# Kernel tuning notes

Hardware: AMD Instinct MI355X
Metric: run time of the kernel (lower is better)

## Reference

```python
import jax, jax.numpy as jnp
import numpy as np

DIM = 512
NUM_HEADS = 8
HEAD_DIM = DIM // NUM_HEADS


def setup_inputs() -> dict:
    key = jax.random.key(0)
    k_x, k_qkv, k_p = jax.random.split(key, 3)
    b, n, c = 8, 4096, DIM
    x = jax.random.normal(k_x, (b, n, c), dtype=jnp.float32)
    # xavier_uniform for Linear(dim, 3*dim): limit = sqrt(6/(in+out))
    lim_qkv = float(np.sqrt(6.0 / (c + 3 * c)))
    w_qkv = jax.random.uniform(k_qkv, (c, 3 * c), dtype=jnp.float32, minval=-lim_qkv, maxval=lim_qkv)
    b_qkv = jnp.zeros((3 * c,), dtype=jnp.float32)
    lim_p = float(np.sqrt(6.0 / (c + c)))
    w_p = jax.random.uniform(k_p, (c, c), dtype=jnp.float32, minval=-lim_p, maxval=lim_p)
    b_p = jnp.zeros((c,), dtype=jnp.float32)
    temperature = jnp.full((NUM_HEADS, 1, 1), 1.0 / np.sqrt(HEAD_DIM), dtype=jnp.float32)
    return {"x": x, "w_qkv": w_qkv, "b_qkv": b_qkv, "w_p": w_p, "b_p": b_p,
            "temperature": temperature}


def reference(x, w_qkv, b_qkv, w_p, b_p, temperature):
    b, n, c = x.shape
    h, d = NUM_HEADS, HEAD_DIM
    qkv = x @ w_qkv + b_qkv                      # [b, n, 3c]
    q, k, v = jnp.split(qkv, 3, axis=-1)         # each [b, n, c]
    # -> [b, h, n, d]
    q = q.reshape(b, n, h, d).transpose(0, 2, 1, 3)
    k = k.reshape(b, n, h, d).transpose(0, 2, 1, 3)
    v = v.reshape(b, n, h, d).transpose(0, 2, 1, 3)
    # channel attention: d x d score matrix, reduced over tokens n
    scores = jnp.einsum('bhnd,bhne->bhde', q, k) * temperature  # [b,h,d,d]
    attn = jax.nn.softmax(scores, axis=-1)
    # y = attn @ v^T then permute -> [b, n, h, d]
    y = jnp.einsum('bhde,bhne->bnhd', attn, v).reshape(b, n, c)
    return y @ w_p + b_p
```

## Files before the change

### kernel.cpp

```cpp
#include <hip/hip_runtime.h>

typedef __attribute__((ext_vector_type(8))) short s16x8;
typedef __attribute__((ext_vector_type(4))) short s16x4;
typedef __attribute__((ext_vector_type(4))) float fx4;

__device__ inline unsigned short f2bf(float f) {
  unsigned u = __float_as_uint(f);
  u += 0x7fffu + ((u >> 16) & 1u);
  return (unsigned short)(u >> 16);
}
__device__ inline float bf2f(unsigned short s) {
  return __uint_as_float(((unsigned)s) << 16);
}

#define GLDS16(gp, lp) \
  __builtin_amdgcn_global_load_lds((const __attribute__((address_space(1))) void*)(gp), \
                                   (__attribute__((address_space(3))) void*)(lp), 16, 0, 0)

__global__ __launch_bounds__(256) void cast_x_k(const float* __restrict__ x,
                                                unsigned short* __restrict__ xb) {
  int i = (blockIdx.x * 256 + threadIdx.x) * 8;
  fx4 a = *(const fx4*)&x[i];
  fx4 b = *(const fx4*)&x[i + 4];
  s16x8 o;
  o[0] = (short)f2bf(a[0]); o[1] = (short)f2bf(a[1]);
  o[2] = (short)f2bf(a[2]); o[3] = (short)f2bf(a[3]);
  o[4] = (short)f2bf(b[0]); o[5] = (short)f2bf(b[1]);
  o[6] = (short)f2bf(b[2]); o[7] = (short)f2bf(b[3]);
  *(s16x8*)&xb[i] = o;
}

__global__ __launch_bounds__(256) void twqkv_k(const float* __restrict__ w,
                                               unsigned short* __restrict__ wT) {
  int o = blockIdx.x * 256 + threadIdx.x;
  int j = o >> 9, kk = o & 511;
  wT[o] = f2bf(w[kk * 1536 + j]);
}

__global__ __launch_bounds__(256) void cast_wp_k(const float* __restrict__ w,
                                                 unsigned short* __restrict__ wb) {
  int o = blockIdx.x * 256 + threadIdx.x;
  wb[o] = f2bf(w[o]);
}

template <int MODE>
__global__ __launch_bounds__(256, 4) void gemm_k(
    const unsigned short* __restrict__ A, const unsigned short* __restrict__ BT,
    const float* __restrict__ bias,
    unsigned short* __restrict__ qo, unsigned short* __restrict__ ko,
    unsigned short* __restrict__ vo, float* __restrict__ outp) {
  __shared__ alignas(16) unsigned short As[2][128 * 32];
  __shared__ alignas(16) unsigned short Bs[2][128 * 32];
  int tid = threadIdx.x, wave = tid >> 6, lane = tid & 63;
  int l15 = lane & 15, l16 = lane >> 4;
  int wr = wave >> 1, wc = wave & 1;

  int nwg = (MODE == 0) ? 3072 : 1024;
  int cpx = nwg >> 3;
  int bid = (blockIdx.x & 7) * cpx + (blockIdx.x >> 3);

  int mt, nt, bb = 0;
  if (MODE == 0) { mt = bid / 12; nt = bid % 12; }
  else { bb = bid >> 7; int r = bid & 127; mt = r >> 2; nt = r & 3; }
  const unsigned short* Ab = A + (MODE == 0 ? (size_t)0 : (size_t)bb * 4096 * 512);
  const unsigned short* Bb = BT + (MODE == 0 ? (size_t)0 : (size_t)bb * 512 * 512);
  int row0 = mt * 128, col0 = nt * 128;

  fx4 acc[4][4];
#pragma unroll
  for (int i = 0; i < 4; ++i)
#pragma unroll
    for (int j = 0; j < 4; ++j) acc[i][j] = (fx4){0.f, 0.f, 0.f, 0.f};

  int smr = wave * 16 + (lane >> 2);
  int skk = (((lane & 3) ^ ((lane >> 3) & 3))) * 8;
  const unsigned short* agp = Ab + (size_t)(row0 + smr) * 512 + skk;
  const unsigned short* bgp = Bb + (size_t)(col0 + smr) * 512 + skk;
  int ldsoff = wave * 512;

#define STAGE(buf, kt_)                                        \
  do {                                                         \
    int k0_ = (kt_) * 32;                                      \
    GLDS16(agp + k0_, &As[buf][ldsoff]);                       \
    GLDS16(agp + 64 * 512 + k0_, &As[buf][ldsoff + 2048]);     \
    GLDS16(bgp + k0_, &Bs[buf][ldsoff]);                       \
    GLDS16(bgp + 64 * 512 + k0_, &Bs[buf][ldsoff + 2048]);     \
  } while (0)

  STAGE(0, 0);
  asm volatile("s_waitcnt vmcnt(0)" ::: "memory");
  __builtin_amdgcn_s_barrier();

  int g = (l15 >> 1) & 3;
  int pa = (l16 ^ g) << 3;

  for (int kt = 0; kt < 16; ++kt) {
    int cur = kt & 1;
    if (kt < 15) STAGE(cur ^ 1, kt + 1);

    s16x8 af[4], bf[4];
#pragma unroll
    for (int mi = 0; mi < 4; ++mi)
      af[mi] = *(const s16x8*)&As[cur][(wr * 64 + mi * 16 + l15) * 32 + pa];
#pragma unroll
    for (int nj = 0; nj < 4; ++nj)
      bf[nj] = *(const s16x8*)&Bs[cur][(wc * 64 + nj * 16 + l15) * 32 + pa];
#pragma unroll
    for (int mi = 0; mi < 4; ++mi)
#pragma unroll
      for (int nj = 0; nj < 4; ++nj)
        acc[mi][nj] = __builtin_amdgcn_mfma_f32_16x16x32_bf16(af[mi], bf[nj], acc[mi][nj], 0, 0, 0);

    asm volatile("s_waitcnt vmcnt(0)" ::: "memory");
    __builtin_amdgcn_s_barrier();
  }
#undef STAGE

  int crow0 = row0 + wr * 64;
  int ccol0 = col0 + wc * 64;
  if (MODE == 0) {
    int seg = ccol0 >> 9;
#pragma unroll
    for (int mi = 0; mi < 4; ++mi)
#pragma unroll
      for (int nj = 0; nj < 4; ++nj) {
        int gc = ccol0 + nj * 16 + l15;
        float bsv = bias[gc];
#pragma unroll
        for (int r = 0; r < 4; ++r) {
          int gr = crow0 + mi * 16 + l16 * 4 + r;
          unsigned short o = f2bf(acc[mi][nj][r] + bsv);
          int b_ = gr >> 12, n_ = gr & 4095;
          if (seg == 0) {
            qo[((((size_t)b_ * 8 + (gc >> 6)) * 4096 + n_) << 6) + (gc & 63)] = o;
          } else if (seg == 1) {
            int c2 = gc - 512;
            ko[((((size_t)b_ * 8 + (c2 >> 6)) * 4096 + n_) << 6) + (c2 & 63)] = o;
          } else {
            vo[((size_t)gr << 9) + (gc - 1024)] = o;
          }
        }
      }
  } else {
#pragma unroll
    for (int mi = 0; mi < 4; ++mi)
#pragma unroll
      for (int nj = 0; nj < 4; ++nj) {
        int gc = ccol0 + nj * 16 + l15;
        float bsv = bias[gc];
#pragma unroll
        for (int r = 0; r < 4; ++r) {
          int gr = crow0 + mi * 16 + l16 * 4 + r;
          outp[(((size_t)bb * 4096 + gr) << 9) + gc] = acc[mi][nj][r] + bsv;
        }
      }
  }
}

__global__ __launch_bounds__(256) void scores_partial_k(const unsigned short* __restrict__ q,
                                                        const unsigned short* __restrict__ k,
                                                        float* __restrict__ sp) {
  __shared__ alignas(16) float qs[64 * 64];
  __shared__ alignas(16) float ks[64 * 64];
  int bid = blockIdx.x;
  int bh = bid >> 3, seg = bid & 7;
  const unsigned short* qb = q + ((size_t)bh * 4096 + seg * 512) * 64;
  const unsigned short* kb = k + ((size_t)bh * 4096 + seg * 512) * 64;
  int tid = threadIdx.x;
  int dg = tid >> 4, eg = tid & 15;
  float acc[4][4] = {{0.f}};
  for (int ch = 0; ch < 8; ++ch) {
    __syncthreads();
    for (int r = 0; r < 4; ++r) {
      int idx = r * 1024 + tid * 4;
      s16x4 qv = *(const s16x4*)&qb[ch * 4096 + idx];
      s16x4 kv = *(const s16x4*)&kb[ch * 4096 + idx];
      fx4 qf = {bf2f((unsigned short)qv[0]), bf2f((unsigned short)qv[1]),
                bf2f((unsigned short)qv[2]), bf2f((unsigned short)qv[3])};
      fx4 kf = {bf2f((unsigned short)kv[0]), bf2f((unsigned short)kv[1]),
                bf2f((unsigned short)kv[2]), bf2f((unsigned short)kv[3])};
      *(fx4*)&qs[idx] = qf;
      *(fx4*)&ks[idx] = kf;
    }
    __syncthreads();
    for (int n = 0; n < 64; ++n) {
      fx4 qv4 = *(const fx4*)&qs[n * 64 + dg * 4];
      fx4 kv4 = *(const fx4*)&ks[n * 64 + eg * 4];
      for (int i = 0; i < 4; ++i)
        for (int j = 0; j < 4; ++j) acc[i][j] += qv4[i] * kv4[j];
    }
  }
  float* o = sp + (size_t)bid * 4096;
  for (int i = 0; i < 4; ++i)
    for (int j = 0; j < 4; ++j) o[(dg * 4 + i) * 64 + eg * 4 + j] = acc[i][j];
}

__global__ __launch_bounds__(256) void softmax_weff_k(const float* __restrict__ sp,
                                                      const unsigned short* __restrict__ wpb,
                                                      const float* __restrict__ temp,
                                                      unsigned short* __restrict__ weffT) {
  __shared__ alignas(16) float S[64 * 64];
  __shared__ alignas(16) unsigned short wps[64 * 128];
  int bh = blockIdx.x >> 2, jblk = blockIdx.x & 3;
  int b = bh >> 3, h = bh & 7;
  int tid = threadIdx.x;
  float tval = temp[h];
  for (int i = tid * 4; i < 4096; i += 1024) {
    fx4 s = {0.f, 0.f, 0.f, 0.f};
    for (int seg = 0; seg < 8; ++seg) {
      fx4 v4 = *(const fx4*)&sp[((size_t)(bh * 8 + seg)) * 4096 + i];
      s += v4;
    }
    s *= tval;
    *(fx4*)&S[i] = s;
  }
  for (int i = tid * 8; i < 8192; i += 2048) {
    int d = i >> 7, c = i & 127;
    *(s16x8*)&wps[i] = *(const s16x8*)&wpb[(size_t)(h * 64 + d) * 512 + jblk * 128 + c];
  }
  __syncthreads();
  if (tid < 64) {
    float* row = &S[tid * 64];
    float mx = row[0];
    for (int e = 1; e < 64; ++e) mx = fmaxf(mx, row[e]);
    float sum = 0.f;
    for (int e = 0; e < 64; ++e) { float p = __expf(row[e] - mx); row[e] = p; sum += p; }
    float inv = 1.f / sum;
    for (int e = 0; e < 64; ++e) row[e] *= inv;
  }
  __syncthreads();
  int jg = tid >> 4, eg = tid & 15;
  int j0 = jg * 8;
  float a[4][8];
  for (int i = 0; i < 4; ++i)
    for (int j = 0; j < 8; ++j) a[i][j] = 0.f;
  for (int d = 0; d < 64; ++d) {
    fx4 at = *(const fx4*)&S[d * 64 + eg * 4];
    s16x8 wv = *(const s16x8*)&wps[d * 128 + j0];
    float wf[8];
    for (int j = 0; j < 8; ++j) wf[j] = bf2f((unsigned short)wv[j]);
    for (int i = 0; i < 4; ++i)
      for (int j = 0; j < 8; ++j) a[i][j] += at[i] * wf[j];
  }
  int jglob = jblk * 128 + j0;
  for (int j = 0; j < 8; ++j)
    for (int i = 0; i < 4; ++i)
      weffT[(((size_t)b * 512 + jglob + j) << 9) + h * 64 + eg * 4 + i] = f2bf(a[i][j]);
}

extern "C" void kernel_launch(void* const* d_in, const int* in_sizes, int n_in,
                              void* d_out, int out_size, void* d_ws, size_t ws_size,
                              hipStream_t stream) {
  const float* x      = (const float*)d_in[0];
  const float* w_qkv  = (const float*)d_in[1];
  const float* b_qkv  = (const float*)d_in[2];
  const float* w_p    = (const float*)d_in[3];
  const float* b_p    = (const float*)d_in[4];
  const float* temp   = (const float*)d_in[5];
  float* out = (float*)d_out;
  char* ws = (char*)d_ws;

  unsigned short* xb    = (unsigned short*)(ws + 0);
  float*          sp    = (float*)(ws + 0);
  unsigned short* weffT = (unsigned short*)(ws + 8388608);
  unsigned short* wqkvT = (unsigned short*)(ws + 33554432);
  unsigned short* wpb   = (unsigned short*)(ws + 35127296);
  unsigned short* qb    = (unsigned short*)(ws + 35651584);
  unsigned short* kb    = (unsigned short*)(ws + 69206016);
  unsigned short* vb    = (unsigned short*)(ws + 102760448);

  cast_x_k<<<8192, 256, 0, stream>>>(x, xb);
  twqkv_k<<<3072, 256, 0, stream>>>(w_qkv, wqkvT);
  cast_wp_k<<<1024, 256, 0, stream>>>(w_p, wpb);
  gemm_k<0><<<3072, 256, 0, stream>>>(xb, wqkvT, b_qkv, qb, kb, vb, nullptr);
  scores_partial_k<<<512, 256, 0, stream>>>(qb, kb, sp);
  softmax_weff_k<<<256, 256, 0, stream>>>(sp, wpb, temp, weffT);
  gemm_k<1><<<1024, 256, 0, stream>>>(vb, weffT, b_p, nullptr, nullptr, nullptr, out);
}
```

Baseline: 171.3 us.

## Reassociate channel attention to avoid materializing Q and V projections

Rewrites the pipeline algebraically. It computes K^T via a GEMM, then X^T K per batch as a split-K GEMM, and forms the scores as Wq^T (X^T K) with bias corrections derived from column sums of x. V is never materialized: softmax·Wp is folded with Wv into a per-batch combined weight, so the final output is a single x @ Wcomb GEMM. The intent is to drop the large Q/V projection GEMMs and their memory traffic. In exchange it adds transposes of x, split-K partial buffers, atomics for the bias terms, and numerics that differ from the original order of operations.

```diff
diff --git a/kernel.cpp b/kernel.cpp
--- a/kernel.cpp
+++ b/kernel.cpp
@@ -18,53 +18,149 @@
                                    (__attribute__((address_space(3))) void*)(lp), 16, 0, 0)
 
 __global__ __launch_bounds__(256) void cast_x_k(const float* __restrict__ x,
-                                                unsigned short* __restrict__ xb) {
-  int i = (blockIdx.x * 256 + threadIdx.x) * 8;
-  fx4 a = *(const fx4*)&x[i];
-  fx4 b = *(const fx4*)&x[i + 4];
-  s16x8 o;
-  o[0] = (short)f2bf(a[0]); o[1] = (short)f2bf(a[1]);
-  o[2] = (short)f2bf(a[2]); o[3] = (short)f2bf(a[3]);
-  o[4] = (short)f2bf(b[0]); o[5] = (short)f2bf(b[1]);
-  o[6] = (short)f2bf(b[2]); o[7] = (short)f2bf(b[3]);
-  *(s16x8*)&xb[i] = o;
-}
-
-__global__ __launch_bounds__(256) void twqkv_k(const float* __restrict__ w,
-                                               unsigned short* __restrict__ wT) {
-  int o = blockIdx.x * 256 + threadIdx.x;
-  int j = o >> 9, kk = o & 511;
-  wT[o] = f2bf(w[kk * 1536 + j]);
-}
-
-__global__ __launch_bounds__(256) void cast_wp_k(const float* __restrict__ w,
-                                                 unsigned short* __restrict__ wb) {
-  int o = blockIdx.x * 256 + threadIdx.x;
-  wb[o] = f2bf(w[o]);
+                                                unsigned short* __restrict__ xb,
+                                                unsigned short* __restrict__ xT,
+                                                float* __restrict__ s_part) {
+  __shared__ unsigned short lt[64 * 66];
+  __shared__ float red[64 * 4];
+  int blk = blockIdx.x;
+  int b = blk >> 9, r = blk & 511, nt = r >> 3, ct = r & 7;
+  int n0 = nt * 64, c0 = ct * 64;
+  int t = threadIdx.x;
+  int rn = t >> 2, seg = (t & 3) * 16;
+  const float* xp = x + ((size_t)b * 4096 + n0 + rn) * 512 + c0 + seg;
+  fx4 v0 = *(const fx4*)&xp[0], v1 = *(const fx4*)&xp[4];
+  fx4 v2 = *(const fx4*)&xp[8], v3 = *(const fx4*)&xp[12];
+  unsigned short h[16];
+  h[0]=f2bf(v0[0]); h[1]=f2bf(v0[1]); h[2]=f2bf(v0[2]); h[3]=f2bf(v0[3]);
+  h[4]=f2bf(v1[0]); h[5]=f2bf(v1[1]); h[6]=f2bf(v1[2]); h[7]=f2bf(v1[3]);
+  h[8]=f2bf(v2[0]); h[9]=f2bf(v2[1]); h[10]=f2bf(v2[2]); h[11]=f2bf(v2[3]);
+  h[12]=f2bf(v3[0]); h[13]=f2bf(v3[1]); h[14]=f2bf(v3[2]); h[15]=f2bf(v3[3]);
+  unsigned short* xbo = xb + ((size_t)b * 4096 + n0 + rn) * 512 + c0 + seg;
+  *(s16x8*)&xbo[0] = *(s16x8*)&h[0];
+  *(s16x8*)&xbo[8] = *(s16x8*)&h[8];
+#pragma unroll
+  for (int k = 0; k < 16; ++k) lt[(seg + k) * 66 + rn] = h[k];
+  __syncthreads();
+  {
+    int c = t & 63, q = t >> 6;
+    float p = 0.f;
+#pragma unroll
+    for (int i = 0; i < 16; ++i) p += bf2f(lt[c * 66 + q * 16 + i]);
+    red[c * 4 + q] = p;
+  }
+  __syncthreads();
+  if (t < 64) {
+    float s = red[t * 4] + red[t * 4 + 1] + red[t * 4 + 2] + red[t * 4 + 3];
+    s_part[((size_t)(b * 64 + nt)) * 512 + c0 + t] = s;
+  }
+  int c = t >> 2, nseg = (t & 3) * 16;
+  unsigned short* xto = xT + ((size_t)b * 512 + c0 + c) * 4096 + n0 + nseg;
+  *(s16x8*)&xto[0] = *(s16x8*)&lt[c * 66 + nseg];
+  *(s16x8*)&xto[8] = *(s16x8*)&lt[c * 66 + nseg + 8];
+}
+
+__global__ __launch_bounds__(256) void wk_t_k(const float* __restrict__ w,
+                                              unsigned short* __restrict__ wkT) {
+  __shared__ unsigned short lt[64 * 66];
+  int blk = blockIdx.x;
+  int rt = blk >> 3, ct = blk & 7;
+  int t = threadIdx.x;
+  int rn = t >> 2, seg = (t & 3) * 16;
+  const float* wp = w + (size_t)(ct * 64 + rn) * 1536 + 512 + rt * 64 + seg;
+#pragma unroll
+  for (int k = 0; k < 16; ++k) lt[(seg + k) * 66 + rn] = f2bf(wp[k]);
+  __syncthreads();
+  int j = t >> 2, nseg = (t & 3) * 16;
+  unsigned short* o = wkT + (size_t)(rt * 64 + j) * 512 + ct * 64 + nseg;
+  *(s16x8*)&o[0] = *(s16x8*)&lt[j * 66 + nseg];
+  *(s16x8*)&o[8] = *(s16x8*)&lt[j * 66 + nseg + 8];
+}
+
+__global__ __launch_bounds__(256) void wvwp_k(const float* __restrict__ w,
+                                              const float* __restrict__ wp,
+                                              unsigned short* __restrict__ wvb,
+                                              unsigned short* __restrict__ wpb) {
+  int blk = blockIdx.x, t = threadIdx.x;
+  if (blk < 128) {
+    int o = blk * 2048 + t * 8;
+    int c = o >> 9, e = o & 511;
+    const float* src = w + (size_t)c * 1536 + 1024 + e;
+    unsigned short h[8];
+#pragma unroll
+    for (int i = 0; i < 8; ++i) h[i] = f2bf(src[i]);
+    *(s16x8*)&wvb[o] = *(s16x8*)&h[0];
+  } else {
+    int o = (blk - 128) * 2048 + t * 8;
+    unsigned short h[8];
+#pragma unroll
+    for (int i = 0; i < 8; ++i) h[i] = f2bf(wp[o + i]);
+    *(s16x8*)&wpb[o] = *(s16x8*)&h[0];
+  }
+}
+
+__global__ __launch_bounds__(256) void ub_k(const float* __restrict__ s_part,
+                                            const float* __restrict__ w,
+                                            const float* __restrict__ b_p,
+                                            float* __restrict__ u,
+                                            float* __restrict__ bias_out) {
+  __shared__ float sb[128];
+  int b = blockIdx.x >> 2, cq = blockIdx.x & 3;
+  int t = threadIdx.x;
+  if (t < 128) {
+    float a = 0.f;
+    for (int nt = 0; nt < 64; ++nt)
+      a += s_part[((size_t)(b * 64 + nt)) * 512 + cq * 128 + t];
+    sb[t] = a;
+  }
+  __syncthreads();
+  float ua0 = 0.f, ua1 = 0.f, ua2 = 0.f, ua3 = 0.f;
+  for (int c = 0; c < 128; ++c) {
+    float sc = sb[c];
+    const float* wr = w + (size_t)(cq * 128 + c) * 1536;
+    ua0 += sc * wr[t];
+    ua1 += sc * wr[t + 256];
+    ua2 += sc * wr[t + 512];
+    ua3 += sc * wr[t + 768];
+  }
+  atomicAdd(&u[b * 1024 + t], ua0);
+  atomicAdd(&u[b * 1024 + t + 256], ua1);
+  atomicAdd(&u[b * 1024 + t + 512], ua2);
+  atomicAdd(&u[b * 1024 + t + 768], ua3);
+  if (cq == 0) {
+    bias_out[b * 512 + t] = b_p[t];
+    bias_out[b * 512 + 256 + t] = b_p[256 + t];
+  }
 }
 
 template <int MODE>
 __global__ __launch_bounds__(256, 4) void gemm_k(
-    const unsigned short* __restrict__ A, const unsigned short* __restrict__ BT,
-    const float* __restrict__ bias,
-    unsigned short* __restrict__ qo, unsigned short* __restrict__ ko,
-    unsigned short* __restrict__ vo, float* __restrict__ outp) {
+    const unsigned short* __restrict__ A0, const unsigned short* __restrict__ B0,
+    const float* __restrict__ bias, unsigned short* __restrict__ obf,
+    float* __restrict__ of32) {
+  constexpr int LD = (MODE == 1) ? 4096 : 512;
+  constexpr int KSTEPS = (MODE == 1) ? 32 : 16;
+  constexpr int NWG = (MODE == 0) ? 1024 : (MODE == 1) ? 512 : (MODE == 2) ? 128 : 1024;
   __shared__ alignas(16) unsigned short As[2][128 * 32];
   __shared__ alignas(16) unsigned short Bs[2][128 * 32];
   int tid = threadIdx.x, wave = tid >> 6, lane = tid & 63;
   int l15 = lane & 15, l16 = lane >> 4;
   int wr = wave >> 1, wc = wave & 1;
 
-  int nwg = (MODE == 0) ? 3072 : 1024;
-  int cpx = nwg >> 3;
-  int bid = (blockIdx.x & 7) * cpx + (blockIdx.x >> 3);
-
-  int mt, nt, bb = 0;
-  if (MODE == 0) { mt = bid / 12; nt = bid % 12; }
-  else { bb = bid >> 7; int r = bid & 127; mt = r >> 2; nt = r & 3; }
-  const unsigned short* Ab = A + (MODE == 0 ? (size_t)0 : (size_t)bb * 4096 * 512);
-  const unsigned short* Bb = BT + (MODE == 0 ? (size_t)0 : (size_t)bb * 512 * 512);
-  int row0 = mt * 128, col0 = nt * 128;
+  int bid = (blockIdx.x & 7) * (NWG >> 3) + (blockIdx.x >> 3);
+  int b = 0, mt = 0, nt = 0, ks = 0;
+  if (MODE == 0) { b = bid >> 7; int r = bid & 127; mt = r >> 5; nt = r & 31; }
+  else if (MODE == 1) { ks = bid >> 7; int r = bid & 127; b = r >> 4; mt = (r >> 2) & 3; nt = r & 3; }
+  else if (MODE == 2) { b = bid >> 4; mt = (bid >> 2) & 3; nt = bid & 3; }
+  else { b = bid >> 7; int r = bid & 127; mt = r >> 2; nt = r & 3; }
+
+  const unsigned short* Ab;
+  const unsigned short* Bb;
+  if (MODE == 0) { Ab = A0 + (size_t)mt * 128 * 512; Bb = B0 + ((size_t)b * 4096 + nt * 128) * 512; }
+  else if (MODE == 1) { Ab = A0 + ((size_t)b * 512 + mt * 128) * 4096 + ks * 1024;
+                        Bb = B0 + ((size_t)b * 512 + nt * 128) * 4096 + ks * 1024; }
+  else if (MODE == 2) { Ab = A0 + ((size_t)b * 512 + mt * 128) * 512; Bb = B0 + (size_t)nt * 128 * 512; }
+  else { Ab = A0 + ((size_t)b * 4096 + mt * 128) * 512; Bb = B0 + ((size_t)b * 512 + nt * 128) * 512; }
 
   fx4 acc[4][4];
 #pragma unroll
@@ -74,17 +170,17 @@
 
   int smr = wave * 16 + (lane >> 2);
   int skk = (((lane & 3) ^ ((lane >> 3) & 3))) * 8;
-  const unsigned short* agp = Ab + (size_t)(row0 + smr) * 512 + skk;
-  const unsigned short* bgp = Bb + (size_t)(col0 + smr) * 512 + skk;
+  const unsigned short* agp = Ab + (size_t)smr * LD + skk;
+  const unsigned short* bgp = Bb + (size_t)smr * LD + skk;
   int ldsoff = wave * 512;
 
-#define STAGE(buf, kt_)                                        \
-  do {                                                         \
-    int k0_ = (kt_) * 32;                                      \
-    GLDS16(agp + k0_, &As[buf][ldsoff]);                       \
-    GLDS16(agp + 64 * 512 + k0_, &As[buf][ldsoff + 2048]);     \
-    GLDS16(bgp + k0_, &Bs[buf][ldsoff]);                       \
-    GLDS16(bgp + 64 * 512 + k0_, &Bs[buf][ldsoff + 2048]);     \
+#define STAGE(buf, kt_)                                          \
+  do {                                                           \
+    int k0_ = (kt_) * 32;                                        \
+    GLDS16(agp + k0_, &As[buf][ldsoff]);                         \
+    GLDS16(agp + (size_t)64 * LD + k0_, &As[buf][ldsoff + 2048]);\
+    GLDS16(bgp + k0_, &Bs[buf][ldsoff]);                         \
+    GLDS16(bgp + (size_t)64 * LD + k0_, &Bs[buf][ldsoff + 2048]);\
   } while (0)
 
   STAGE(0, 0);
@@ -94,9 +190,9 @@
   int g = (l15 >> 1) & 3;
   int pa = (l16 ^ g) << 3;
 
-  for (int kt = 0; kt < 16; ++kt) {
+  for (int kt = 0; kt < KSTEPS; ++kt) {
     int cur = kt & 1;
-    if (kt < 15) STAGE(cur ^ 1, kt + 1);
+    if (kt < KSTEPS - 1) STAGE(cur ^ 1, kt + 1);
 
     s16x8 af[4], bf[4];
 #pragma unroll
@@ -116,136 +212,123 @@
   }
 #undef STAGE
 
-  int crow0 = row0 + wr * 64;
-  int ccol0 = col0 + wc * 64;
-  if (MODE == 0) {
-    int seg = ccol0 >> 9;
-#pragma unroll
-    for (int mi = 0; mi < 4; ++mi)
-#pragma unroll
-      for (int nj = 0; nj < 4; ++nj) {
-        int gc = ccol0 + nj * 16 + l15;
-        float bsv = bias[gc];
-#pragma unroll
-        for (int r = 0; r < 4; ++r) {
-          int gr = crow0 + mi * 16 + l16 * 4 + r;
-          unsigned short o = f2bf(acc[mi][nj][r] + bsv);
-          int b_ = gr >> 12, n_ = gr & 4095;
-          if (seg == 0) {
-            qo[((((size_t)b_ * 8 + (gc >> 6)) * 4096 + n_) << 6) + (gc & 63)] = o;
-          } else if (seg == 1) {
-            int c2 = gc - 512;
-            ko[((((size_t)b_ * 8 + (c2 >> 6)) * 4096 + n_) << 6) + (c2 & 63)] = o;
-          } else {
-            vo[((size_t)gr << 9) + (gc - 1024)] = o;
-          }
+  int R0 = mt * 128 + wr * 64, C0 = nt * 128 + wc * 64;
+#pragma unroll
+  for (int mi = 0; mi < 4; ++mi)
+#pragma unroll
+    for (int nj = 0; nj < 4; ++nj) {
+      int gc = C0 + nj * 16 + l15;
+#pragma unroll
+      for (int r = 0; r < 4; ++r) {
+        int gr = R0 + mi * 16 + l16 * 4 + r;
+        float val = acc[mi][nj][r];
+        if (MODE == 0) {
+          obf[((size_t)(b * 512 + gr)) * 4096 + gc] = f2bf(val + bias[gr]);
+        } else if (MODE == 1) {
+          of32[((size_t)((ks * 8 + b) * 512 + gr)) * 512 + gc] = val;
+        } else if (MODE == 2) {
+          obf[((size_t)(b * 512 + gr)) * 512 + gc] = f2bf(val);
+        } else {
+          of32[((size_t)(b * 4096 + gr)) * 512 + gc] = val + bias[b * 512 + gc];
         }
       }
-  } else {
-#pragma unroll
-    for (int mi = 0; mi < 4; ++mi)
-#pragma unroll
-      for (int nj = 0; nj < 4; ++nj) {
-        int gc = ccol0 + nj * 16 + l15;
-        float bsv = bias[gc];
-#pragma unroll
-        for (int r = 0; r < 4; ++r) {
-          int gr = crow0 + mi * 16 + l16 * 4 + r;
-          outp[(((size_t)bb * 4096 + gr) << 9) + gc] = acc[mi][nj][r] + bsv;
-        }
-      }
-  }
-}
-
-__global__ __launch_bounds__(256) void scores_partial_k(const unsigned short* __restrict__ q,
-                                                        const unsigned short* __restrict__ k,
-                                                        float* __restrict__ sp) {
-  __shared__ alignas(16) float qs[64 * 64];
-  __shared__ alignas(16) float ks[64 * 64];
-  int bid = blockIdx.x;
-  int bh = bid >> 3, seg = bid & 7;
-  const unsigned short* qb = q + ((size_t)bh * 4096 + seg * 512) * 64;
-  const unsigned short* kb = k + ((size_t)bh * 4096 + seg * 512) * 64;
+    }
+}
+
+__global__ __launch_bounds__(256) void scores_k(
+    const float* __restrict__ Ppart, const float* __restrict__ w_qkv,
+    const float* __restrict__ b_qkv, const float* __restrict__ u,
+    const float* __restrict__ temp, const unsigned short* __restrict__ wpb,
+    unsigned short* __restrict__ weffT, float* __restrict__ bias_out) {
+  __shared__ alignas(16) float Ps[64 * 64];
+  __shared__ alignas(16) float Ws[64 * 64];
+  __shared__ alignas(16) float Ss[64 * 64];
+  __shared__ alignas(16) unsigned short wps[64 * 128];
+  int bh = blockIdx.x;
+  int b = bh >> 3, h = bh & 7;
   int tid = threadIdx.x;
   int dg = tid >> 4, eg = tid & 15;
   float acc[4][4] = {{0.f}};
-  for (int ch = 0; ch < 8; ++ch) {
+  for (int cch = 0; cch < 8; ++cch) {
     __syncthreads();
-    for (int r = 0; r < 4; ++r) {
-      int idx = r * 1024 + tid * 4;
-      s16x4 qv = *(const s16x4*)&qb[ch * 4096 + idx];
-      s16x4 kv = *(const s16x4*)&kb[ch * 4096 + idx];
-      fx4 qf = {bf2f((unsigned short)qv[0]), bf2f((unsigned short)qv[1]),
-                bf2f((unsigned short)qv[2]), bf2f((unsigned short)qv[3])};
-      fx4 kf = {bf2f((unsigned short)kv[0]), bf2f((unsigned short)kv[1]),
-                bf2f((unsigned short)kv[2]), bf2f((unsigned short)kv[3])};
-      *(fx4*)&qs[idx] = qf;
-      *(fx4*)&ks[idx] = kf;
+    for (int p = 0; p < 4; ++p) {
+      int idx = p * 1024 + tid * 4;
+      int cr = idx >> 6, ce = idx & 63;
+      size_t base = ((size_t)(cch * 64 + cr)) * 512 + h * 64 + ce;
+      fx4 v = {0.f, 0.f, 0.f, 0.f};
+#pragma unroll
+      for (int kk = 0; kk < 4; ++kk)
+        v += *(const fx4*)&Ppart[(size_t)(kk * 8 + b) * 262144 + base];
+      *(fx4*)&Ps[idx] = v;
+      *(fx4*)&Ws[idx] = *(const fx4*)&w_qkv[(size_t)(cch * 64 + cr) * 1536 + h * 64 + ce];
     }
     __syncthreads();
-    for (int n = 0; n < 64; ++n) {
-      fx4 qv4 = *(const fx4*)&qs[n * 64 + dg * 4];
-      fx4 kv4 = *(const fx4*)&ks[n * 64 + eg * 4];
+    for (int cc = 0; cc < 64; ++cc) {
+      fx4 wv = *(const fx4*)&Ws[cc * 64 + dg * 4];
+      fx4 pv = *(const fx4*)&Ps[cc * 64 + eg * 4];
+#pragma unroll
       for (int i = 0; i < 4; ++i)
-        for (int j = 0; j < 4; ++j) acc[i][j] += qv4[i] * kv4[j];
-    }
-  }
-  float* o = sp + (size_t)bid * 4096;
+#pragma unroll
+        for (int j = 0; j < 4; ++j) acc[i][j] += wv[i] * pv[j];
+    }
+  }
+  float tval = temp[h];
+  __syncthreads();
+#pragma unroll
   for (int i = 0; i < 4; ++i)
-    for (int j = 0; j < 4; ++j) o[(dg * 4 + i) * 64 + eg * 4 + j] = acc[i][j];
-}
-
-__global__ __launch_bounds__(256) void softmax_weff_k(const float* __restrict__ sp,
-                                                      const unsigned short* __restrict__ wpb,
-                                                      const float* __restrict__ temp,
-                                                      unsigned short* __restrict__ weffT) {
-  __shared__ alignas(16) float S[64 * 64];
-  __shared__ alignas(16) unsigned short wps[64 * 128];
-  int bh = blockIdx.x >> 2, jblk = blockIdx.x & 3;
-  int b = bh >> 3, h = bh & 7;
-  int tid = threadIdx.x;
-  float tval = temp[h];
-  for (int i = tid * 4; i < 4096; i += 1024) {
-    fx4 s = {0.f, 0.f, 0.f, 0.f};
-    for (int seg = 0; seg < 8; ++seg) {
-      fx4 v4 = *(const fx4*)&sp[((size_t)(bh * 8 + seg)) * 4096 + i];
-      s += v4;
-    }
-    s *= tval;
-    *(fx4*)&S[i] = s;
-  }
-  for (int i = tid * 8; i < 8192; i += 2048) {
-    int d = i >> 7, c = i & 127;
-    *(s16x8*)&wps[i] = *(const s16x8*)&wpb[(size_t)(h * 64 + d) * 512 + jblk * 128 + c];
-  }
+#pragma unroll
+    for (int j = 0; j < 4; ++j) {
+      int d = dg * 4 + i, e = eg * 4 + j;
+      float ksum = u[b * 1024 + 512 + h * 64 + e] + 4096.0f * b_qkv[512 + h * 64 + e];
+      Ss[d * 64 + e] = (acc[i][j] + b_qkv[h * 64 + d] * ksum) * tval;
+    }
   __syncthreads();
   if (tid < 64) {
-    float* row = &S[tid * 64];
+    float* row = &Ss[tid * 64];
     float mx = row[0];
     for (int e = 1; e < 64; ++e) mx = fmaxf(mx, row[e]);
     float sum = 0.f;
-    for (int e = 0; e < 64; ++e) { float p = __expf(row[e] - mx); row[e] = p; sum += p; }
+    for (int e = 0; e < 64; ++e) { float pv = __expf(row[e] - mx); row[e] = pv; sum += pv; }
     float inv = 1.f / sum;
     for (int e = 0; e < 64; ++e) row[e] *= inv;
   }
   __syncthreads();
-  int jg = tid >> 4, eg = tid & 15;
+  int jg = tid & 15, egr = tid >> 4;
   int j0 = jg * 8;
-  float a[4][8];
-  for (int i = 0; i < 4; ++i)
-    for (int j = 0; j < 8; ++j) a[i][j] = 0.f;
-  for (int d = 0; d < 64; ++d) {
-    fx4 at = *(const fx4*)&S[d * 64 + eg * 4];
-    s16x8 wv = *(const s16x8*)&wps[d * 128 + j0];
-    float wf[8];
-    for (int j = 0; j < 8; ++j) wf[j] = bf2f((unsigned short)wv[j]);
+  for (int jc = 0; jc < 4; ++jc) {
+    __syncthreads();
+    for (int i = tid * 8; i < 8192; i += 2048) {
+      int dd = i >> 7, c = i & 127;
+      *(s16x8*)&wps[i] = *(const s16x8*)&wpb[(size_t)(h * 64 + dd) * 512 + jc * 128 + c];
+    }
+    __syncthreads();
+    float a[4][8];
+#pragma unroll
     for (int i = 0; i < 4; ++i)
-      for (int j = 0; j < 8; ++j) a[i][j] += at[i] * wf[j];
-  }
-  int jglob = jblk * 128 + j0;
-  for (int j = 0; j < 8; ++j)
-    for (int i = 0; i < 4; ++i)
-      weffT[(((size_t)b * 512 + jglob + j) << 9) + h * 64 + eg * 4 + i] = f2bf(a[i][j]);
+#pragma unroll
+      for (int j = 0; j < 8; ++j) a[i][j] = 0.f;
+    for (int dd = 0; dd < 64; ++dd) {
+      fx4 at = *(const fx4*)&Ss[dd * 64 + egr * 4];
+      s16x8 wv = *(const s16x8*)&wps[dd * 128 + j0];
+      float wf[8];
+#pragma unroll
+      for (int j = 0; j < 8; ++j) wf[j] = bf2f((unsigned short)wv[j]);
+#pragma unroll
+      for (int i = 0; i < 4; ++i)
+#pragma unroll
+        for (int j = 0; j < 8; ++j) a[i][j] += at[i] * wf[j];
+    }
+#pragma unroll
+    for (int j = 0; j < 8; ++j) {
+      float cb = 0.f;
+#pragma unroll
+      for (int i = 0; i < 4; ++i) {
+        weffT[((size_t)b * 512 + jc * 128 + j0 + j) * 512 + h * 64 + egr * 4 + i] = f2bf(a[i][j]);
+        cb += b_qkv[1024 + h * 64 + egr * 4 + i] * a[i][j];
+      }
+      atomicAdd(&bias_out[b * 512 + jc * 128 + j0 + j], cb);
+    }
+  }
 }
 
 extern "C" void kernel_launch(void* const* d_in, const int* in_sizes, int n_in,
@@ -260,20 +343,27 @@
   float* out = (float*)d_out;
   char* ws = (char*)d_ws;
 
-  unsigned short* xb    = (unsigned short*)(ws + 0);
-  float*          sp    = (float*)(ws + 0);
-  unsigned short* weffT = (unsigned short*)(ws + 8388608);
-  unsigned short* wqkvT = (unsigned short*)(ws + 33554432);
-  unsigned short* wpb   = (unsigned short*)(ws + 35127296);
-  unsigned short* qb    = (unsigned short*)(ws + 35651584);
-  unsigned short* kb    = (unsigned short*)(ws + 69206016);
-  unsigned short* vb    = (unsigned short*)(ws + 102760448);
-
-  cast_x_k<<<8192, 256, 0, stream>>>(x, xb);
-  twqkv_k<<<3072, 256, 0, stream>>>(w_qkv, wqkvT);
-  cast_wp_k<<<1024, 256, 0, stream>>>(w_p, wpb);
-  gemm_k<0><<<3072, 256, 0, stream>>>(xb, wqkvT, b_qkv, qb, kb, vb, nullptr);
-  scores_partial_k<<<512, 256, 0, stream>>>(qb, kb, sp);
-  softmax_weff_k<<<256, 256, 0, stream>>>(sp, wpb, temp, weffT);
-  gemm_k<1><<<1024, 256, 0, stream>>>(vb, weffT, b_p, nullptr, nullptr, nullptr, out);
-}
+  unsigned short* xb     = (unsigned short*)(ws + 0);
+  unsigned short* xT     = (unsigned short*)(ws + 33554432);
+  unsigned short* kT     = (unsigned short*)(ws + 67108864);
+  float*          Ppart  = (float*)(ws + 100663296);
+  float*          s_part = (float*)(ws + 100663296);
+  unsigned short* wkT    = (unsigned short*)(ws + 134217728);
+  unsigned short* wvb    = (unsigned short*)(ws + 134742016);
+  unsigned short* wpb    = (unsigned short*)(ws + 135266304);
+  float*          u      = (float*)(ws + 135790592);
+  float*          bias_o = (float*)(ws + 135823360);
+  unsigned short* weffT  = (unsigned short*)(ws + 33554432);
+  unsigned short* wcombT = (unsigned short*)(ws + 37748736);
+
+  hipMemsetAsync(u, 0, 32768, stream);
+  cast_x_k<<<4096, 256, 0, stream>>>(x, xb, xT, s_part);
+  wk_t_k<<<64, 256, 0, stream>>>(w_qkv, wkT);
+  wvwp_k<<<256, 256, 0, stream>>>(w_qkv, w_p, wvb, wpb);
+  ub_k<<<32, 256, 0, stream>>>(s_part, w_qkv, b_p, u, bias_o);
+  gemm_k<0><<<1024, 256, 0, stream>>>(wkT, xb, b_qkv + 512, kT, nullptr);
+  gemm_k<1><<<512, 256, 0, stream>>>(xT, kT, nullptr, nullptr, Ppart);
+  scores_k<<<64, 256, 0, stream>>>(Ppart, w_qkv, b_qkv, u, temp, wpb, weffT, bias_o);
+  gemm_k<2><<<128, 256, 0, stream>>>(weffT, wvb, nullptr, wcombT, nullptr);
+  gemm_k<3><<<1024, 256, 0, stream>>>(xb, wcombT, bias_o, nullptr, out);
+}
```

Result: slower. 272.0 us (+58.7%).
